# Performance work log

Measured on AMD Instinct MI355X. Metric: run time of the kernel, lower is better.

## Reference

```python
import jax, jax.numpy as jnp
import numpy as np


def _cdist(queries, data):
    # Euclidean distance matrix [m, n], matching torch.cdist(p=2)
    q2 = jnp.sum(queries * queries, axis=1)[:, None]
    d2 = jnp.sum(data * data, axis=1)[None, :]
    sq = q2 + d2 - 2.0 * (queries @ data.T)
    return jnp.sqrt(jnp.maximum(sq, 0.0))


def setup_inputs() -> dict:
    key = jax.random.key(0)
    k1, k2 = jax.random.split(key)
    data = jax.random.normal(k1, (16384, 3), dtype=jnp.float32)
    queries = jax.random.normal(k2, (16384, 3), dtype=jnp.float32)
    return {"data": data, "queries": queries, "n_neigbor": 32}


def reference(data, queries, n_neigbor):
    m = queries.shape[0]
    n = data.shape[0]
    dists = _cdist(queries, data)                      # [m, n]
    sorted_dist = jnp.sort(dists, axis=1)              # full row sort, as in original
    k = sorted_dist[:, n_neigbor]                      # (n_neigbor)-th smallest distance
    in_nbr = dists < k[:, None]                        # strictly-less -> exactly n_neigbor True per row (no ties)
    # nonzero() in the original emits column indices in ascending order per row.
    # Replicate with fixed shapes: map non-neighbors to sentinel n, sort, keep first n_neigbor.
    cols = jnp.where(in_nbr, jnp.arange(n, dtype=jnp.int64)[None, :], jnp.int64(n))
    neighbors_index = jnp.sort(cols, axis=1)[:, :n_neigbor].reshape(-1)  # [m * n_neigbor]
    counts = jnp.sum(in_nbr.astype(jnp.int64), axis=1)
    splits = jnp.concatenate([jnp.zeros((1,), dtype=jnp.int64), jnp.cumsum(counts)])  # [m+1]
    return neighbors_index, splits
```

## Files before the change

### kernel.cpp

```cpp
#include <hip/hip_runtime.h>
#include <stdint.h>

typedef unsigned long long u64;
typedef unsigned int u32;

#define NQ 16384
#define ND 16384
#define KNB 32
#define KK 33
#define SPLITS_BASE (NQ * KNB)
#define CAP 512
#define NRR (CAP / 64)
#define NWQ 2
#define G 36
#define G3 (G*G*G)
#define SCB ((G3 + 255) / 256)
#define FINF (__int_as_float(0x7f800000))


template<int BITS>
__device__ __forceinline__ int wave_sum_small(int v) {
    int tot = 0;
    #pragma unroll
    for (int b = 0; b < BITS; ++b)
        tot += (int)__popcll(__ballot((v >> b) & 1)) << b;
    return tot;
}
__device__ __forceinline__ float wave_max_f(float v) {
    #pragma unroll
    for (int s = 1; s < 64; s <<= 1) v = fmaxf(v, __shfl_xor(v, s, 64));
    return v;
}
__device__ __forceinline__ int wave_excl_prefix(int v, int lane) {
    int x = v;
    #pragma unroll
    for (int s = 1; s < 64; s <<= 1) {
        const int y = __shfl_up(x, s, 64);
        if (lane >= s) x += y;
    }
    return x - v;
}
__device__ __forceinline__ int iclamp(int v, int lo, int hi) {
    return v < lo ? lo : (v > hi ? hi : v);
}
__device__ __forceinline__ u32 fenc(float f) {
    const u32 u = __float_as_uint(f);
    return (u & 0x80000000u) ? ~u : (u | 0x80000000u);
}
__device__ __forceinline__ float fdec(u32 e) {
    const u32 u = (e & 0x80000000u) ? (e & 0x7fffffffu) : ~e;
    return __uint_as_float(u);
}

__device__ __forceinline__ float bisect_rank8(const float (&r)[NRR], int rank) {
    u32 lo = 0u, hi = 0x7f800000u;
    #pragma unroll 1
    while (lo < hi) {
        const u32 mid = (lo + hi) >> 1;
        const float pv = __uint_as_float(mid);
        int c = 0;
        #pragma unroll
        for (int j = 0; j < NRR; ++j) c += (r[j] <= pv) ? 1 : 0;
        const int tot = wave_sum_small<4>(c);
        if (tot >= rank) hi = mid; else lo = mid + 1;
    }
    return __uint_as_float(hi);
}

__device__ __forceinline__ void pool_prune(float* kp, u32* ip, int& cnt, float& Tk,
                                           int lane, u64 lt) {
    float m = FINF;
    #pragma unroll 1
    for (int j = lane; j < cnt; j += 64) m = fminf(m, kp[j]);
    const float M = wave_max_f(m);
    int nc = 0;
    #pragma unroll 1
    for (int j0 = 0; j0 < cnt; j0 += 64) {
        const int j = j0 + lane;
        const bool val = j < cnt;
        float k = FINF; u32 id = 0;
        if (val) { k = kp[j]; id = ip[j]; }
        const bool keep = val && (k <= M);
        const u64 mask = __ballot(keep);
        if (keep) {
            const int s = nc + (int)__popcll(mask & lt);
            kp[s] = k; ip[s] = id;
        }
        nc += (int)__popcll(mask);
    }
    cnt = nc; Tk = M;
}

__device__ __forceinline__ void pool_hard_prune(float* kp, u32* ip, int& cnt,
                                                int lane, u64 lt) {
    float r[NRR];
    #pragma unroll
    for (int j = 0; j < NRR; ++j) {
        const int s = j * 64 + lane;
        r[j] = (s < cnt) ? kp[s] : FINF;
    }
    const float v = bisect_rank8(r, 64);
    int nc = 0, eqs = 0;
    #pragma unroll 1
    for (int j0 = 0; j0 < cnt; j0 += 64) {
        const int j = j0 + lane;
        const bool val = j < cnt;
        float k = FINF; u32 id = 0;
        if (val) { k = kp[j]; id = ip[j]; }
        const bool lt_v = val && (k < v);
        const bool eq_v = val && (k == v);
        const u64 mlt = __ballot(lt_v);
        const u64 meq = __ballot(eq_v);
        const int poplt = (int)__popcll(mlt);
        const int popeq = (int)__popcll(meq);
        if (lt_v) { const int s = nc + (int)__popcll(mlt & lt); kp[s] = k; ip[s] = id; }
        if (eq_v) {
            const int pe = (int)__popcll(meq & lt);
            if (eqs + pe < 64) { const int s = nc + poplt + pe; kp[s] = k; ip[s] = id; }
        }
        int kept_eq = popeq;
        if (eqs + popeq > 64) kept_eq = (64 - eqs > 0) ? (64 - eqs) : 0;
        nc += poplt + kept_eq;
        eqs += popeq;
    }
    cnt = nc;
}

__device__ __forceinline__ void grid_geom(const u32* bbe, float& mnx, float& mny, float& mnz,
                                          float& hx, float& hy, float& hz) {
    mnx = fdec(bbe[0]); mny = fdec(bbe[1]); mnz = fdec(bbe[2]);
    const float mxx = -fdec(bbe[3]), mxy = -fdec(bbe[4]), mxz = -fdec(bbe[5]);
    hx = fmaxf((mxx - mnx) * (1.0f / G), 1e-20f);
    hy = fmaxf((mxy - mny) * (1.0f / G), 1e-20f);
    hz = fmaxf((mxz - mnz) * (1.0f / G), 1e-20f);
}

__device__ __forceinline__ u32 cell_of(const u32* bbe, float x, float y, float z) {
    float mnx, mny, mnz, hx, hy, hz;
    grid_geom(bbe, mnx, mny, mnz, hx, hy, hz);
    const int cx = iclamp((int)((x - mnx) / hx), 0, G-1);
    const int cy = iclamp((int)((y - mny) / hy), 0, G-1);
    const int cz = iclamp((int)((z - mnz) / hz), 0, G-1);
    return (u32)((cz * G + cy) * G + cx);
}

__global__ __launch_bounds__(256) void bbox_kernel(const float* __restrict__ data,
                                                   u32* __restrict__ bbe,
                                                   u32* __restrict__ hist) {
    const int i = blockIdx.x * 256 + threadIdx.x;
    for (int h = i; h < G3; h += ND) hist[h] = 0u;
    const int lane = threadIdx.x & 63;
    const float x = data[3*i], y = data[3*i+1], z = data[3*i+2];
    float mnx = x, mny = y, mnz = z, nx = -x, ny = -y, nz = -z;
    #pragma unroll
    for (int s = 1; s < 64; s <<= 1) {
        mnx = fminf(mnx, __shfl_xor(mnx, s, 64)); nx = fminf(nx, __shfl_xor(nx, s, 64));
        mny = fminf(mny, __shfl_xor(mny, s, 64)); ny = fminf(ny, __shfl_xor(ny, s, 64));
        mnz = fminf(mnz, __shfl_xor(mnz, s, 64)); nz = fminf(nz, __shfl_xor(nz, s, 64));
    }
    if (lane == 0) {
        atomicMin(&bbe[0], fenc(mnx)); atomicMin(&bbe[1], fenc(mny)); atomicMin(&bbe[2], fenc(mnz));
        atomicMin(&bbe[3], fenc(nx));  atomicMin(&bbe[4], fenc(ny));  atomicMin(&bbe[5], fenc(nz));
    }
}

__global__ __launch_bounds__(256) void cellid_hist(const float* __restrict__ data,
                                                   const u32* __restrict__ bbe,
                                                   u32* __restrict__ hist) {
    const int i = blockIdx.x * 256 + threadIdx.x;
    atomicAdd(&hist[cell_of(bbe, data[3*i], data[3*i+1], data[3*i+2])], 1u);
}

__global__ __launch_bounds__(256) void scan_partial(const u32* __restrict__ hist,
                                                    u32* __restrict__ cstart,
                                                    u32* __restrict__ bsum) {
    __shared__ u32 lds[256];
    const int t = threadIdx.x;
    const int i = blockIdx.x * 256 + t;
    const u32 v = (i < G3) ? hist[i] : 0u;
    lds[t] = v;
    __syncthreads();
    u32 x = v;
    for (int off = 1; off < 256; off *= 2) {
        const u32 add = (t >= off) ? lds[t - off] : 0u;
        __syncthreads();
        x += add; lds[t] = x;
        __syncthreads();
    }
    if (i < G3) cstart[i] = x - v;
    if (t == 255) bsum[blockIdx.x] = x;
}

__global__ __launch_bounds__(256) void scan_add(u32* __restrict__ cstart,
                                                u32* __restrict__ cursor,
                                                const u32* __restrict__ bsum) {
    __shared__ u32 lds[256];
    const int t = threadIdx.x;
    const u32 bv = (t < SCB) ? bsum[t] : 0u;
    lds[t] = bv;
    __syncthreads();
    u32 y = bv;
    for (int off = 1; off < 256; off *= 2) {
        const u32 add = (t >= off) ? lds[t - off] : 0u;
        __syncthreads();
        y += add; lds[t] = y;
        __syncthreads();
    }
    const u32 excl = lds[blockIdx.x] - ((blockIdx.x < SCB) ? bsum[blockIdx.x] : 0u);
    __syncthreads();
    const int i = blockIdx.x * 256 + t;
    if (i < G3) {
        const u32 val = cstart[i] + excl;
        cstart[i] = val; cursor[i] = val;
    }
    if (i == 0) cstart[G3] = (u32)ND;
}

__global__ __launch_bounds__(256) void scatter(const float* __restrict__ data,
                                               const u32* __restrict__ bbe,
                                               u32* __restrict__ cursor,
                                               float4* __restrict__ pts) {
    const int i = blockIdx.x * 256 + threadIdx.x;
    const float x = data[3*i], y = data[3*i+1], z = data[3*i+2];
    const u32 pos = atomicAdd(&cursor[cell_of(bbe, x, y, z)], 1u);
    pts[pos] = make_float4(x, y, z, __uint_as_float((u32)i));
}

__global__ __launch_bounds__(64 * NWQ) void knn_grid(const float4* __restrict__ pts,
                                                     const u32* __restrict__ cstart,
                                                     const float* __restrict__ queries,
                                                     const u32* __restrict__ bbe,
                                                     int* __restrict__ out_nb,
                                                     int* __restrict__ splits) {
    __shared__ float keyP[NWQ][CAP];
    __shared__ u32   idxP[NWQ][CAP];
    __shared__ int   accI[NWQ][KNB];

    const int lane = threadIdx.x & 63;
    const int wid  = threadIdx.x >> 6;
    const int q = blockIdx.x * NWQ + wid;
    const u64 lt = (1ull << lane) - 1ull;
    float* kp = keyP[wid];
    u32*   ip = idxP[wid];

    const float qx = queries[3*q], qy = queries[3*q+1], qz = queries[3*q+2];
    const float q2 = __fadd_rn(__fadd_rn(__fmul_rn(qx,qx), __fmul_rn(qy,qy)), __fmul_rn(qz,qz));

    float mnx, mny, mnz, hx, hy, hz;
    grid_geom(bbe, mnx, mny, mnz, hx, hy, hz);
    const float hmin = fminf(hx, fminf(hy, hz));
    const int cx = iclamp((int)((qx - mnx) / hx), 0, G-1);
    const int cy = iclamp((int)((qy - mny) / hy), 0, G-1);
    const int cz = iclamp((int)((qz - mnz) / hz), 0, G-1);

    float Tk = FINF;
    int cnt = 0;

    auto gather_batch = [&](int sA, int lA, int sB, int lB) {
        const int len = lA + lB;
        const int P = wave_excl_prefix(len, lane);
        const int T = __shfl(P + len, 63, 64);
        #pragma unroll 1
        for (int g0 = 0; g0 < T; g0 += 64) {
            const int pos = g0 + lane;
            const bool val = pos < T;
            int rsel = 0;
            #pragma unroll
            for (int st = 32; st >= 1; st >>= 1) {
                const int t = rsel + st;
                const int Pt = __shfl(P, t, 64);
                if (Pt <= pos) rsel = t;
            }
            const int Pr  = __shfl(P,  rsel, 64);
            const int sAr = __shfl(sA, rsel, 64);
            const int lAr = __shfl(lA, rsel, 64);
            const int sBr = __shfl(sB, rsel, 64);
            const int off = pos - Pr;
            const int pi = (off < lAr) ? (sAr + off) : (sBr + (off - lAr));
            float key = FINF; u32 oi = 0; bool acc = false;
            if (val) {
                const float4 w = pts[pi];
                oi = __float_as_uint(w.w);
                const float d2 = __fadd_rn(__fadd_rn(__fmul_rn(w.x,w.x), __fmul_rn(w.y,w.y)),
                                           __fmul_rn(w.z,w.z));
                const float dot = __fmaf_rn(qz, w.z, __fmaf_rn(qy, w.y, __fmul_rn(qx, w.x)));
                const float sq  = __fsub_rn(__fadd_rn(q2, d2), __fadd_rn(dot, dot));
                key = fmaxf(sq, 0.0f);
                acc = key <= Tk;
            }
            const u64 mask = __ballot(acc);
            if (mask) {
                if (acc) {
                    const int s = cnt + (int)__popcll(mask & lt);
                    kp[s] = key; ip[s] = oi;
                }
                cnt += (int)__popcll(mask);
                if (cnt > CAP - 64) {
                    pool_prune(kp, ip, cnt, Tk, lane, lt);
                    if (cnt > CAP - 64) pool_hard_prune(kp, ip, cnt, lane, lt);
                }
            }
        }
    };

    int W = 0;
    {
        int ccount = 0;
        while (ccount < KK && W < G) {
            ++W;
            const int side = 2*W + 1, nrows = side * side;
            ccount = 0;
            for (int r0 = 0; r0 < nrows; r0 += 64) {
                const int rid = r0 + lane;
                int len = 0;
                if (rid < nrows) {
                    const int dz = rid / side - W, dy = rid % side - W;
                    const int zz = cz + dz, yy = cy + dy;
                    if (zz >= 0 && zz < G && yy >= 0 && yy < G) {
                        const int xlo = cx - W < 0 ? 0 : cx - W;
                        const int xhi = cx + W > G-1 ? G-1 : cx + W;
                        const int rb = (zz * G + yy) * G;
                        len = (int)cstart[rb + xhi + 1] - (int)cstart[rb + xlo];
                    }
                }
                ccount += wave_sum_small<6>(len < 63 ? len : 63);
            }
        }
    }

    {
        const int side = 2*W + 1, nrows = side * side;
        for (int r0 = 0; r0 < nrows; r0 += 64) {
            const int rid = r0 + lane;
            int sA = 0, lA = 0;
            if (rid < nrows) {
                const int dz = rid / side - W, dy = rid % side - W;
                const int zz = cz + dz, yy = cy + dy;
                if (zz >= 0 && zz < G && yy >= 0 && yy < G) {
                    const int xlo = cx - W < 0 ? 0 : cx - W;
                    const int xhi = cx + W > G-1 ? G-1 : cx + W;
                    const int rb = (zz * G + yy) * G;
                    sA = (int)cstart[rb + xlo];
                    lA = (int)cstart[rb + xhi + 1] - sA;
                }
            }
            gather_batch(sA, lA, 0, 0);
        }
    }

    float k33b;
    if (cnt <= 64) {
        float v = (lane < cnt) ? kp[lane] : FINF;
        #pragma unroll
        for (int k = 2; k <= 64; k <<= 1) {
            #pragma unroll
            for (int j = k >> 1; j >= 1; j >>= 1) {
                const float o = __shfl_xor(v, j, 64);
                const bool up = ((lane & k) == 0);
                const bool keepmin = (((lane & j) == 0) == up);
                v = keepmin ? fminf(v, o) : fmaxf(v, o);
            }
        }
        k33b = __shfl(v, KK - 1, 64);
    } else {
        float r[NRR];
        #pragma unroll
        for (int j = 0; j < NRR; ++j) {
            const int s = j * 64 + lane;
            r[j] = (s < cnt) ? kp[s] : FINF;
        }
        k33b = bisect_rank8(r, KK);
    }

    {
        int nc = 0;
        #pragma unroll 1
        for (int j0 = 0; j0 < cnt; j0 += 64) {
            const int j = j0 + lane;
            const bool val = j < cnt;
            float k = FINF; u32 id = 0;
            if (val) { k = kp[j]; id = ip[j]; }
            const bool keep = val && (k <= k33b);
            const u64 mask = __ballot(keep);
            if (keep) {
                const int s = nc + (int)__popcll(mask & lt);
                kp[s] = k; ip[s] = id;
            }
            nc += (int)__popcll(mask);
        }
        cnt = nc; Tk = k33b;
    }

    const float R2m = __fmaf_rn(k33b, 1.0002f, 1e-3f);
    if (!(R2m < (float)W * (float)W * hmin * hmin)) {
        const float Rm = sqrtf(R2m);
        const int Dz = (int)fminf(floorf(Rm / hz) + 1.0f, (float)G);
        const int Dy = (int)fminf(floorf(Rm / hy) + 1.0f, (float)G);
        const int sidey = 2*Dy + 1;
        const int nrows = (2*Dz + 1) * sidey;
        for (int r0 = 0; r0 < nrows; r0 += 64) {
            const int rid = r0 + lane;
            int sA = 0, lA = 0, sB = 0, lB = 0;
            if (rid < nrows) {
                const int dz = rid / sidey - Dz;
                const int dy = rid % sidey - Dy;
                const int zz = cz + dz, yy = cy + dy;
                if (zz >= 0 && zz < G && yy >= 0 && yy < G) {
                    const int adz = dz < 0 ? -dz : dz;
                    const int ady = dy < 0 ? -dy : dy;
                    const float mz = (adz >= 1) ? (float)(adz - 1) * hz : 0.0f;
                    const float my = (ady >= 1) ? (float)(ady - 1) * hy : 0.0f;
                    const float rowmin2 = mz*mz + my*my;
                    if (rowmin2 <= R2m) {
                        const int dxr = (int)fminf(floorf(sqrtf(R2m - rowmin2) / hx) + 1.0f, (float)G);
                        const int xlo = cx - dxr < 0 ? 0 : cx - dxr;
                        const int xhi = cx + dxr > G-1 ? G-1 : cx + dxr;
                        if (xlo <= xhi) {
                            const int rb = (zz * G + yy) * G;
                            if (adz <= W && ady <= W) {
                                const int xhiA = (cx - W - 1 < xhi) ? cx - W - 1 : xhi;
                                const int xloB = (cx + W + 1 > xlo) ? cx + W + 1 : xlo;
                                if (xlo <= xhiA) {
                                    sA = (int)cstart[rb + xlo];
                                    lA = (int)cstart[rb + xhiA + 1] - sA;
                                }
                                if (xloB <= xhi) {
                                    sB = (int)cstart[rb + xloB];
                                    lB = (int)cstart[rb + xhi + 1] - sB;
                                }
                            } else {
                                sA = (int)cstart[rb + xlo];
                                lA = (int)cstart[rb + xhi + 1] - sA;
                            }
                        }
                    }
                }
            }
            gather_batch(sA, lA, sB, lB);
        }
    }

    float k33;
    if (cnt <= 64) {
        float v = (lane < cnt) ? kp[lane] : FINF;
        #pragma unroll
        for (int k = 2; k <= 64; k <<= 1) {
            #pragma unroll
            for (int j = k >> 1; j >= 1; j >>= 1) {
                const float o = __shfl_xor(v, j, 64);
                const bool up = ((lane & k) == 0);
                const bool keepmin = (((lane & j) == 0) == up);
                v = keepmin ? fminf(v, o) : fmaxf(v, o);
            }
        }
        k33 = __shfl(v, KK - 1, 64);
    } else {
        float r[NRR];
        #pragma unroll
        for (int j = 0; j < NRR; ++j) {
            const int s = j * 64 + lane;
            r[j] = (s < cnt) ? kp[s] : FINF;
        }
        k33 = bisect_rank8(r, KK);
    }

    const float kd = sqrtf(k33);
    float cut;
    if (!(kd > 0.0f)) {
        cut = -1.0f;
    } else {
        int bi = __float_as_int(__fmul_rn(kd, kd));
        #pragma unroll 1
        for (int s = 0; s < 8; ++s) {
            if (bi > 0 && sqrtf(__int_as_float(bi - 1)) >= kd) --bi; else break;
        }
        #pragma unroll 1
        for (int s = 0; s < 8; ++s) {
            if (sqrtf(__int_as_float(bi)) < kd) ++bi; else break;
        }
        cut = __int_as_float(bi);
    }

    int c = 0;
    #pragma unroll 1
    for (int j0 = 0; j0 < cnt; j0 += 64) {
        const int j = j0 + lane;
        const bool val = j < cnt;
        const float k = val ? kp[j] : FINF;
        const bool keep = val && (k < cut);
        const u64 mask = __ballot(keep);
        if (keep) {
            const int s = c + (int)__popcll(mask & lt);
            if (s < KNB) accI[wid][s] = (int)ip[j];
        }
        c += (int)__popcll(mask);
    }
    if (c > KNB) c = KNB;

    if (lane < KNB) {
        if (lane < c) {
            const int my = accI[wid][lane];
            int rank = 0;
            #pragma unroll 1
            for (int j = 0; j < KNB; ++j)
                if (j < c) rank += (accI[wid][j] < my) ? 1 : 0;
            out_nb[(size_t)q * KNB + rank] = my;
        } else {
            out_nb[(size_t)q * KNB + lane] = ND;
        }
    }
    if (lane == 0) splits[1 + q] = c;
}

__global__ __launch_bounds__(256) void knn_direct_kernel(const float* __restrict__ data,
                                                         const float* __restrict__ queries,
                                                         int* __restrict__ out_nb,
                                                         int* __restrict__ splits) {
    __shared__ float4 tile[1024];
    const int q = blockIdx.x * 256 + threadIdx.x;
    const float qx = queries[3*q], qy = queries[3*q+1], qz = queries[3*q+2];
    const float q2 = __fadd_rn(__fadd_rn(__fmul_rn(qx,qx), __fmul_rn(qy,qy)), __fmul_rn(qz,qz));
    float arrk[KK]; int arri[KK];
    for (int j = 0; j < KK; ++j) { arrk[j] = FINF; arri[j] = ND; }
    float cur_maxk = FINF;
    for (int t0 = 0; t0 < ND; t0 += 1024) {
        for (int p = threadIdx.x; p < 1024; p += 256) {
            const int g = t0 + p;
            const float x = data[3*g], y = data[3*g+1], z = data[3*g+2];
            const float d2 = __fadd_rn(__fadd_rn(__fmul_rn(x,x), __fmul_rn(y,y)), __fmul_rn(z,z));
            tile[p] = make_float4(x, y, z, d2);
        }
        __syncthreads();
        for (int p = 0; p < 1024; ++p) {
            const float4 dp = tile[p];
            const float dot = __fmaf_rn(qz, dp.z, __fmaf_rn(qy, dp.y, __fmul_rn(qx, dp.x)));
            const float sq  = __fsub_rn(__fadd_rn(q2, dp.w), __fadd_rn(dot, dot));
            const float key = fmaxf(sq, 0.0f);
            if (key < cur_maxk) {
                int mp = 0; float m = -1.0f;
                for (int j = 0; j < KK; ++j) if (arrk[j] > m) { m = arrk[j]; mp = j; }
                arrk[mp] = key; arri[mp] = t0 + p;
                m = -1.0f;
                for (int j = 0; j < KK; ++j) if (arrk[j] > m) m = arrk[j];
                cur_maxk = m;
            }
        }
        __syncthreads();
    }
    const float kdist = sqrtf(cur_maxk);
    int acc[KNB]; int c = 0;
    for (int j = 0; j < KK; ++j) {
        const float d = sqrtf(arrk[j]);
        if (d < kdist && c < KNB) acc[c++] = arri[j];
    }
    for (int a = 1; a < c; ++a) {
        const int v = acc[a]; int j = a;
        while (j > 0 && acc[j-1] > v) { acc[j] = acc[j-1]; --j; }
        acc[j] = v;
    }
    int* row = out_nb + (size_t)q * KNB;
    for (int j = 0; j < KNB; ++j) row[j] = (j < c) ? acc[j] : ND;
    splits[1 + q] = c;
}

__global__ __launch_bounds__(1024) void splits_scan_kernel(int* __restrict__ splits) {
    __shared__ int lds[1024];
    const int t = threadIdx.x;
    int v[16]; int s = 0;
    #pragma unroll
    for (int j = 0; j < 16; ++j) { v[j] = splits[1 + t*16 + j]; s += v[j]; }
    lds[t] = s;
    __syncthreads();
    for (int off = 1; off < 1024; off *= 2) {
        const int add = (t >= off) ? lds[t - off] : 0;
        __syncthreads();
        lds[t] += add;
        __syncthreads();
    }
    int run = lds[t] - s;
    #pragma unroll
    for (int j = 0; j < 16; ++j) { run += v[j]; splits[1 + t*16 + j] = run; }
    if (t == 0) splits[0] = 0;
}

extern "C" void kernel_launch(void* const* d_in, const int* in_sizes, int n_in,
                              void* d_out, int out_size, void* d_ws, size_t ws_size,
                              hipStream_t stream) {
    const float* data    = (const float*)d_in[0];
    const float* queries = (const float*)d_in[1];
    int* out    = (int*)d_out;
    int* splits = out + SPLITS_BASE;

    const size_t bb_off     = 0;
    const size_t hist_off   = 64;
    const size_t cstart_off = hist_off + (size_t)G3 * 4;
    const size_t cursor_off = cstart_off + (size_t)(G3 + 1) * 4;
    const size_t bsum_off   = cursor_off + (size_t)G3 * 4;
    size_t pts_off          = bsum_off + 256 * 4;
    pts_off = (pts_off + 255) & ~(size_t)255;
    const size_t need       = pts_off + (size_t)ND * 16;

    if (ws_size >= need) {
        u32*    bbe    = (u32*)((char*)d_ws + bb_off);
        u32*    hist   = (u32*)((char*)d_ws + hist_off);
        u32*    cstart = (u32*)((char*)d_ws + cstart_off);
        u32*    cursor = (u32*)((char*)d_ws + cursor_off);
        u32*    bsum   = (u32*)((char*)d_ws + bsum_off);
        float4* pts    = (float4*)((char*)d_ws + pts_off);

        hipMemsetAsync(bbe, 0xFF, 24, stream);
        hipLaunchKernelGGL(bbox_kernel, dim3(ND / 256), dim3(256), 0, stream, data, bbe, hist);
        hipLaunchKernelGGL(cellid_hist, dim3(ND / 256), dim3(256), 0, stream, data, bbe, hist);
        hipLaunchKernelGGL(scan_partial, dim3(SCB), dim3(256), 0, stream, hist, cstart, bsum);
        hipLaunchKernelGGL(scan_add, dim3(SCB), dim3(256), 0, stream, cstart, cursor, bsum);
        hipLaunchKernelGGL(scatter, dim3(ND / 256), dim3(256), 0, stream, data, bbe, cursor, pts);
        hipLaunchKernelGGL(knn_grid, dim3(NQ / NWQ), dim3(64 * NWQ), 0, stream,
                           pts, cstart, queries, bbe, out, splits);
    } else {
        hipLaunchKernelGGL(knn_direct_kernel, dim3(NQ / 256), dim3(256), 0, stream,
                           data, queries, out, splits);
    }
    hipLaunchKernelGGL(splits_scan_kernel, dim3(1), dim3(1024), 0, stream, splits);
}
```

Before: 111.7 us.

## Grow search shells incrementally and select k-th via 128-wide bitonic sort

Replaces the separate count pass followed by a full-cube gather with a single loop that gathers only the new shell of cells at each radius until at least 33 candidates are pooled. This removes the redundant counting traversal and avoids re-reading inner cells. Selection of the 33rd smallest distance now prunes the pool and uses a two-register 128-element bitonic sort when the pool fits, falling back to bisection otherwise. Risks include extra prune passes and the larger sort network adding shuffle work.

Result: slower. 118.9 us (+6.5%).

```diff
diff --git a/kernel.cpp b/kernel.cpp
--- a/kernel.cpp
+++ b/kernel.cpp
@@ -65,6 +65,27 @@
         if (tot >= rank) hi = mid; else lo = mid + 1;
     }
     return __uint_as_float(hi);
+}
+
+__device__ __forceinline__ void bitonic128(float& v0, float& v1, int lane) {
+    #pragma unroll
+    for (int k = 2; k <= 128; k <<= 1) {
+        #pragma unroll
+        for (int j = k >> 1; j >= 1; j >>= 1) {
+            if (j >= 64) {
+                const float a = fminf(v0, v1), b = fmaxf(v0, v1);
+                v0 = a; v1 = b;
+            } else {
+                const float o0 = __shfl_xor(v0, j, 64);
+                const float o1 = __shfl_xor(v1, j, 64);
+                const bool bj = ((lane & j) == 0);
+                const bool up0 = (k == 128) ? true : ((lane & k) == 0);
+                const bool up1 = (k == 128) ? true : ((k == 64) ? false : ((lane & k) == 0));
+                v0 = (bj == up0) ? fminf(v0, o0) : fmaxf(v0, o0);
+                v1 = (bj == up1) ? fminf(v1, o1) : fmaxf(v1, o1);
+            }
+        }
+    }
 }
 
 __device__ __forceinline__ void pool_prune(float* kp, u32* ip, int& cnt, float& Tk,
@@ -303,74 +324,55 @@
         }
     };
 
-    int W = 0;
-    {
-        int ccount = 0;
-        while (ccount < KK && W < G) {
-            ++W;
-            const int side = 2*W + 1, nrows = side * side;
-            ccount = 0;
-            for (int r0 = 0; r0 < nrows; r0 += 64) {
-                const int rid = r0 + lane;
-                int len = 0;
-                if (rid < nrows) {
-                    const int dz = rid / side - W, dy = rid % side - W;
-                    const int zz = cz + dz, yy = cy + dy;
-                    if (zz >= 0 && zz < G && yy >= 0 && yy < G) {
-                        const int xlo = cx - W < 0 ? 0 : cx - W;
-                        const int xhi = cx + W > G-1 ? G-1 : cx + W;
-                        const int rb = (zz * G + yy) * G;
-                        len = (int)cstart[rb + xhi + 1] - (int)cstart[rb + xlo];
-                    }
-                }
-                ccount += wave_sum_small<6>(len < 63 ? len : 63);
-            }
-        }
-    }
-
-    {
-        const int side = 2*W + 1, nrows = side * side;
-        for (int r0 = 0; r0 < nrows; r0 += 64) {
-            const int rid = r0 + lane;
-            int sA = 0, lA = 0;
-            if (rid < nrows) {
-                const int dz = rid / side - W, dy = rid % side - W;
-                const int zz = cz + dz, yy = cy + dy;
-                if (zz >= 0 && zz < G && yy >= 0 && yy < G) {
-                    const int xlo = cx - W < 0 ? 0 : cx - W;
-                    const int xhi = cx + W > G-1 ? G-1 : cx + W;
-                    const int rb = (zz * G + yy) * G;
-                    sA = (int)cstart[rb + xlo];
-                    lA = (int)cstart[rb + xhi + 1] - sA;
-                }
-            }
-            gather_batch(sA, lA, 0, 0);
-        }
-    }
-
-    float k33b;
-    if (cnt <= 64) {
-        float v = (lane < cnt) ? kp[lane] : FINF;
-        #pragma unroll
-        for (int k = 2; k <= 64; k <<= 1) {
-            #pragma unroll
-            for (int j = k >> 1; j >= 1; j >>= 1) {
-                const float o = __shfl_xor(v, j, 64);
-                const bool up = ((lane & k) == 0);
-                const bool keepmin = (((lane & j) == 0) == up);
-                v = keepmin ? fminf(v, o) : fmaxf(v, o);
-            }
-        }
-        k33b = __shfl(v, KK - 1, 64);
-    } else {
+    auto select33 = [&]() -> float {
+        int guard = 0;
+        while (cnt > 128 && guard < 2) { pool_prune(kp, ip, cnt, Tk, lane, lt); ++guard; }
+        if (cnt <= 128) {
+            float v0 = (lane < cnt) ? kp[lane] : FINF;
+            float v1 = (64 + lane < cnt) ? kp[64 + lane] : FINF;
+            bitonic128(v0, v1, lane);
+            return __shfl(v0, KK - 1, 64);
+        }
         float r[NRR];
         #pragma unroll
         for (int j = 0; j < NRR; ++j) {
             const int s = j * 64 + lane;
             r[j] = (s < cnt) ? kp[s] : FINF;
         }
-        k33b = bisect_rank8(r, KK);
-    }
+        return bisect_rank8(r, KK);
+    };
+
+    int W = -1;
+    while (cnt < KK && W < G) {
+        ++W;
+        const int side = 2*W + 1, nrows = side * side;
+        for (int r0 = 0; r0 < nrows; r0 += 64) {
+            const int rid = r0 + lane;
+            int sA = 0, lA = 0, sB = 0, lB = 0;
+            if (rid < nrows) {
+                const int dz = rid / side - W, dy = rid % side - W;
+                const int zz = cz + dz, yy = cy + dy;
+                if (zz >= 0 && zz < G && yy >= 0 && yy < G) {
+                    const int adz = dz < 0 ? -dz : dz;
+                    const int ady = dy < 0 ? -dy : dy;
+                    const int rb = (zz * G + yy) * G;
+                    if (adz == W || ady == W) {
+                        const int xlo = cx - W < 0 ? 0 : cx - W;
+                        const int xhi = cx + W > G-1 ? G-1 : cx + W;
+                        sA = (int)cstart[rb + xlo];
+                        lA = (int)cstart[rb + xhi + 1] - sA;
+                    } else {
+                        const int xl = cx - W, xr = cx + W;
+                        if (xl >= 0)   { sA = (int)cstart[rb + xl]; lA = (int)cstart[rb + xl + 1] - sA; }
+                        if (xr <= G-1) { sB = (int)cstart[rb + xr]; lB = (int)cstart[rb + xr + 1] - sB; }
+                    }
+                }
+            }
+            gather_batch(sA, lA, sB, lB);
+        }
+    }
+
+    const float k33b = select33();
 
     {
         int nc = 0;
@@ -440,29 +442,7 @@
         }
     }
 
-    float k33;
-    if (cnt <= 64) {
-        float v = (lane < cnt) ? kp[lane] : FINF;
-        #pragma unroll
-        for (int k = 2; k <= 64; k <<= 1) {
-            #pragma unroll
-            for (int j = k >> 1; j >= 1; j >>= 1) {
-                const float o = __shfl_xor(v, j, 64);
-                const bool up = ((lane & k) == 0);
-                const bool keepmin = (((lane & j) == 0) == up);
-                v = keepmin ? fminf(v, o) : fmaxf(v, o);
-            }
-        }
-        k33 = __shfl(v, KK - 1, 64);
-    } else {
-        float r[NRR];
-        #pragma unroll
-        for (int j = 0; j < NRR; ++j) {
-            const int s = j * 64 + lane;
-            r[j] = (s < cnt) ? kp[s] : FINF;
-        }
-        k33 = bisect_rank8(r, KK);
-    }
+    const float k33 = select33();
 
     const float kd = sqrtf(k33);
     float cut;
```
